# Kernel optimization log

Hardware: AMD Instinct MI355X
Metric: run time of the kernel (lower is better)

Reference implementation:

```python
import jax, jax.numpy as jnp
import numpy as np

NUM_HEADS = 16
ROPE_THETA = 10000.0


def _rope_cos_sin(head_dim, seq_len, theta=ROPE_THETA):
    # matches precompute_freqs_cis: theta ** (-(2i)/head_dim)
    exps = -(jnp.arange(0, head_dim, 2)[: head_dim // 2].astype(jnp.float32)) / head_dim
    freqs = theta ** exps                                   # [hd/2]
    ang = jnp.arange(seq_len, dtype=jnp.float32)[:, None] * freqs[None, :]  # [S, hd/2]
    return jnp.cos(ang), jnp.sin(ang)


def _apply_rope(x, cos, sin):
    # x: [B, H, S, hd]; interpret consecutive pairs as complex numbers
    x2 = x.reshape(*x.shape[:-1], -1, 2)
    xr, xi = x2[..., 0], x2[..., 1]
    c = cos[None, None]  # [1,1,S,hd/2]
    s = sin[None, None]
    outr = xr * c - xi * s
    outi = xr * s + xi * c
    return jnp.stack([outr, outi], axis=-1).reshape(x.shape)


def setup_inputs() -> dict:
    key = jax.random.key(0)
    ks = jax.random.split(key, 9)
    B, S, D = 2, 2048, 1024
    scale = 0.02
    x = jax.random.normal(ks[0], (B, S, D), jnp.float32)
    Wq = jax.random.normal(ks[1], (D, D), jnp.float32) * scale
    bq = jax.random.normal(ks[2], (D,), jnp.float32) * scale
    Wk = jax.random.normal(ks[3], (D, D), jnp.float32) * scale
    bk = jax.random.normal(ks[4], (D,), jnp.float32) * scale
    Wv = jax.random.normal(ks[5], (D, D), jnp.float32) * scale
    bv = jax.random.normal(ks[6], (D,), jnp.float32) * scale
    Wo = jax.random.normal(ks[7], (D, D), jnp.float32) * scale
    return {"x": x, "Wq": Wq, "bq": bq, "Wk": Wk, "bk": bk,
            "Wv": Wv, "bv": bv, "Wo": Wo}


def reference(x, Wq, bq, Wk, bk, Wv, bv, Wo):
    B, S, D = x.shape
    H = NUM_HEADS
    hd = D // H
    # projections (torch Linear: x @ W.T + b), split heads -> [B,H,S,hd]
    q = (x @ Wq.T + bq).reshape(B, S, H, hd).transpose(0, 2, 1, 3)
    k = (x @ Wk.T + bk).reshape(B, S, H, hd).transpose(0, 2, 1, 3)
    v = (x @ Wv.T + bv).reshape(B, S, H, hd).transpose(0, 2, 1, 3)
    cos, sin = _rope_cos_sin(hd, S)
    q = _apply_rope(q, cos, sin)
    k = _apply_rope(k, cos, sin)
    # NOTE: original scales by sqrt(input_dim), not sqrt(head_dim)
    inv_scale = 1.0 / jnp.sqrt(jnp.asarray(D, jnp.float32))
    scores = jax.nn.softmax(jnp.einsum('bhqd,bhkd->bhqk', q, k) * inv_scale, axis=-1)
    out = jnp.einsum('bhqk,bhkd->bhqd', scores, v)
    out = out.transpose(0, 2, 1, 3).reshape(B, S, D)
    return out @ Wo.T
```

## Files before the change

kernel.cpp:

```cpp
#include <hip/hip_runtime.h>
#include <math.h>

namespace {
constexpr int kB = 2;
constexpr int kS = 2048;
constexpr int kD = 1024;
constexpr int kH = 16;
constexpr int kHD = 64;
constexpr int kBS = kB * kS;
constexpr float kInvScale = 0.03125f;
constexpr float kQScale = 0.03125f * 1.4426950408889634f;
constexpr int BM = 128, BN = 64, BK = 64;
}

typedef __attribute__((ext_vector_type(8))) short short8;
typedef __attribute__((ext_vector_type(4))) float f32x4;
typedef __attribute__((ext_vector_type(4))) unsigned short u16x4;
typedef __attribute__((ext_vector_type(4))) unsigned int u32x4;

__device__ inline unsigned short f2bf(float f) {
  union { float f; unsigned u; } v;
  v.f = f;
  unsigned r = v.u + 0x7FFFu + ((v.u >> 16) & 1u);
  return (unsigned short)(r >> 16);
}

__device__ inline unsigned pack_bf16_pair(float lo, float hi) {
  union { float f; unsigned u; } a, b;
  a.f = hi; b.f = lo;
  return __builtin_amdgcn_perm(a.u + 0x8000u, b.u + 0x8000u, 0x07060302u);
}

__device__ inline void gload_lds16(const unsigned short* g, unsigned short* l) {
  __builtin_amdgcn_global_load_lds(
      (const __attribute__((address_space(1))) void*)g,
      (__attribute__((address_space(3))) void*)l, 16, 0, 0);
}

__global__ __launch_bounds__(256) void cast_prep_kernel(
    const float* __restrict__ x, const float* __restrict__ Wq,
    const float* __restrict__ Wk, const float* __restrict__ Wv,
    const float* __restrict__ Wo, unsigned short* __restrict__ xb,
    unsigned short* __restrict__ wb, float2* __restrict__ rope) {
  const int tid = blockIdx.x * 256 + threadIdx.x;
  const int stride = gridDim.x * 256;
  for (int i = tid; i < 1048576; i += stride) {
    const float* src;
    unsigned short* dst;
    int off;
    if (i < 524288) {
      src = x; dst = xb; off = i;
    } else {
      const int j = i - 524288;
      const int w = j >> 17;
      src = (w == 0) ? Wq : (w == 1) ? Wk : (w == 2) ? Wv : Wo;
      dst = wb + (size_t)w * (kD * kD);
      off = j & 131071;
    }
    const float4 a = reinterpret_cast<const float4*>(src)[off * 2];
    const float4 b = reinterpret_cast<const float4*>(src)[off * 2 + 1];
    short8 o;
    o[0] = (short)f2bf(a.x); o[1] = (short)f2bf(a.y);
    o[2] = (short)f2bf(a.z); o[3] = (short)f2bf(a.w);
    o[4] = (short)f2bf(b.x); o[5] = (short)f2bf(b.y);
    o[6] = (short)f2bf(b.z); o[7] = (short)f2bf(b.w);
    reinterpret_cast<short8*>(dst)[off] = o;
  }
  for (int i = tid; i < kS * 32; i += stride) {
    const int s = i >> 5;
    const int pr = i & 31;
    const float f = powf(10000.0f, -(float)pr / 32.0f);
    const float ang = (float)s * f;
    rope[i] = make_float2(cosf(ang), sinf(ang));
  }
}

__global__ __launch_bounds__(256) void gemm_bt_kernel(
    const unsigned short* __restrict__ A, const unsigned short* __restrict__ Wb,
    const float* __restrict__ bq, const float* __restrict__ bk,
    const float* __restrict__ bv, const float2* __restrict__ rope,
    unsigned short* __restrict__ qo, unsigned short* __restrict__ ko,
    unsigned short* __restrict__ vo, float* __restrict__ outp, int mode_base) {
  const int mode = mode_base + blockIdx.z;
  const unsigned short* __restrict__ W = Wb + (size_t)mode * (kD * kD);
  const int rt = blockIdx.x * BM;
  const int ct = blockIdx.y * BN;
  const int t = threadIdx.x;
  const int wv = t >> 6;
  const int lane = t & 63;
  const int l15 = lane & 15;
  const int lg = lane >> 4;
  const int wr = wv >> 1;
  const int wc = wv & 1;

  __shared__ unsigned short As[BM * BK];
  __shared__ unsigned short Bs[BN * BK];

  f32x4 acc[4][2];
#pragma unroll
  for (int m = 0; m < 4; ++m)
#pragma unroll
    for (int n = 0; n < 2; ++n) acc[m][n] = f32x4{0.f, 0.f, 0.f, 0.f};

  for (int kt = 0; kt < kD / BK; ++kt) {
    const int k0 = kt * BK;
    __syncthreads();
#pragma unroll
    for (int i = 0; i < 4; ++i) {
      const int off = wv * 4096 + i * 1024;
      const int p = off + lane * 16;
      const int row = p >> 7;
      const int src = ((p >> 4) & 7) ^ (row & 7);
      gload_lds16(A + (size_t)(rt + row) * kD + k0 + src * 8, As + off / 2);
    }
#pragma unroll
    for (int i = 0; i < 2; ++i) {
      const int off = wv * 2048 + i * 1024;
      const int p = off + lane * 16;
      const int row = p >> 7;
      const int src = ((p >> 4) & 7) ^ (row & 7);
      gload_lds16(W + (size_t)(ct + row) * kD + k0 + src * 8, Bs + off / 2);
    }
    __syncthreads();

#pragma unroll
    for (int ks = 0; ks < 2; ++ks) {
      short8 af[4], bf[2];
#pragma unroll
      for (int m = 0; m < 4; ++m) {
        const int row = wr * 64 + m * 16 + l15;
        const int chunk = (ks * 4 + lg) ^ (row & 7);
        af[m] = *reinterpret_cast<const short8*>(&As[row * BK + chunk * 8]);
      }
#pragma unroll
      for (int n = 0; n < 2; ++n) {
        const int row = wc * 32 + n * 16 + l15;
        const int chunk = (ks * 4 + lg) ^ (row & 7);
        bf[n] = *reinterpret_cast<const short8*>(&Bs[row * BK + chunk * 8]);
      }
      __builtin_amdgcn_s_setprio(1);
#pragma unroll
      for (int m = 0; m < 4; ++m)
#pragma unroll
        for (int n = 0; n < 2; ++n)
          acc[m][n] = __builtin_amdgcn_mfma_f32_16x16x32_bf16(
              af[m], bf[n], acc[m][n], 0, 0, 0);
      __builtin_amdgcn_s_setprio(0);
    }
  }

#pragma unroll
  for (int m = 0; m < 4; ++m) {
    const int grow0 = rt + wr * 64 + m * 16 + lg * 4;
    const int bb = grow0 >> 11;
    const int s0 = grow0 & (kS - 1);
#pragma unroll
    for (int n = 0; n < 2; ++n) {
      const int gcol = ct + wc * 32 + n * 16 + l15;
      if (mode == 3) {
#pragma unroll
        for (int reg = 0; reg < 4; ++reg)
          outp[(size_t)(grow0 + reg) * kD + gcol] = acc[m][n][reg];
      } else if (mode == 2) {
        const float bsv = bv[gcol];
        const int h = gcol >> 6, d = gcol & 63;
        u16x4 o;
#pragma unroll
        for (int reg = 0; reg < 4; ++reg)
          o[reg] = f2bf(acc[m][n][reg] + bsv);
        *reinterpret_cast<u16x4*>(
            &vo[((size_t)(bb * kH + h) * kHD + d) * kS + s0]) = o;
      } else {
        const float bsv = (mode == 0) ? bq[gcol] : bk[gcol];
        const float post = (mode == 0) ? kQScale : 1.0f;
        unsigned short* __restrict__ dst = (mode == 0) ? qo : ko;
        const int h = gcol >> 6, d = gcol & 63;
        const int pr = d >> 1;
        const float sgn = (d & 1) ? 1.0f : -1.0f;
#pragma unroll
        for (int reg = 0; reg < 4; ++reg) {
          const int s = s0 + reg;
          const float val = acc[m][n][reg] + bsv;
          const float par = __shfl_xor(val, 1);
          const float2 cs = rope[s * 32 + pr];
          const float o = (val * cs.x + par * cs.y * sgn) * post;
          dst[((size_t)(bb * kH + h) * kS + s) * kHD + d] = f2bf(o);
        }
      }
    }
  }
}

__global__ __launch_bounds__(512) void attn_mfma_kernel(
    const unsigned short* __restrict__ qb, const unsigned short* __restrict__ kb,
    const unsigned short* __restrict__ vtb, unsigned short* __restrict__ attn) {
  const int qt = blockIdx.x;
  const int h = blockIdx.y;
  const int b = blockIdx.z;
  const int t = threadIdx.x;
  const int wave = t >> 6;
  const int lane = t & 63;
  const int l15 = lane & 15;
  const int lg = lane >> 4;
  const int g = wave >> 2;
  const int st = wave & 3;

  __shared__ __align__(16) unsigned char smem[2 * 16384 + 2 * 16384 + 512];
  unsigned short* Ks0 = (unsigned short*)smem;
  unsigned short* Vs0 = (unsigned short*)(smem + 32768);
  float* Ocomb = (float*)smem;
  float* lcomb = (float*)(smem + 65536);

  const size_t bh = (size_t)(b * kH + h);
  const unsigned short* qp = qb + bh * kS * kHD;
  const unsigned short* kp = kb + bh * kS * kHD;
  const unsigned short* vp = vtb + bh * (size_t)kHD * kS;

  const int qrow0 = qt * 128 + st * 32;

  short8 qf[2][2];
#pragma unroll
  for (int qi = 0; qi < 2; ++qi)
#pragma unroll
    for (int f = 0; f < 2; ++f)
      qf[qi][f] = *reinterpret_cast<const short8*>(
          qp + (size_t)(qrow0 + qi * 16 + l15) * kHD + f * 32 + lg * 8);

  short8 ones;
#pragma unroll
  for (int j = 0; j < 8; ++j) ones[j] = (short)0x3F80;

  f32x4 acc_o[2][4], acc_l[2];
#pragma unroll
  for (int qi = 0; qi < 2; ++qi) {
    acc_l[qi] = f32x4{0.f, 0.f, 0.f, 0.f};
#pragma unroll
    for (int ot = 0; ot < 4; ++ot) acc_o[qi][ot] = f32x4{0.f, 0.f, 0.f, 0.f};
  }

  const int srow = t >> 3;
  const int sc = (t & 7) ^ (srow & 7);
  const int kvrow = (srow & 0x23) | ((srow & 0x0C) << 1) | ((srow & 0x10) >> 2);
  const int ldsoff = wave * 512;

#pragma unroll
  for (int hh = 0; hh < 2; ++hh) {
    gload_lds16(kp + (size_t)(hh * 64 + kvrow) * kHD + sc * 8,
                &Ks0[hh * 4096 + ldsoff]);
    gload_lds16(vp + (size_t)srow * kS + hh * 64 + sc * 8,
                &Vs0[hh * 4096 + ldsoff]);
  }
  __syncthreads();

  constexpr int NT = kS / 128;
  for (int kt = 0; kt < NT; ++kt) {
    const int cur = kt & 1;
    unsigned short* Ksb = Ks0 + cur * 8192;
    unsigned short* Vsb = Vs0 + cur * 8192;
    if (kt + 1 < NT) {
      const int nb = (kt + 1) * 128;
#pragma unroll
      for (int hh = 0; hh < 2; ++hh) {
        gload_lds16(kp + (size_t)(nb + hh * 64 + kvrow) * kHD + sc * 8,
                    &Ks0[(cur ^ 1) * 8192 + hh * 4096 + ldsoff]);
        gload_lds16(vp + (size_t)srow * kS + nb + hh * 64 + sc * 8,
                    &Vs0[(cur ^ 1) * 8192 + hh * 4096 + ldsoff]);
      }
    }

#pragma unroll
    for (int hh = 0; hh < 2; ++hh) {
      unsigned short* Ksc = Ksb + hh * 4096;
      unsigned short* Vsc = Vsb + hh * 4096;

      short8 kf[2][2], vf[4];
#pragma unroll
      for (int nt = 0; nt < 2; ++nt) {
        const int row = g * 32 + nt * 16 + l15;
#pragma unroll
        for (int f = 0; f < 2; ++f) {
          const int c = (f * 4 + lg) ^ (row & 7);
          kf[nt][f] = *reinterpret_cast<const short8*>(&Ksc[row * 64 + c * 8]);
        }
      }
#pragma unroll
      for (int ot = 0; ot < 4; ++ot) {
        const int row = ot * 16 + l15;
        const int c = (4 * g + lg) ^ (row & 7);
        vf[ot] = *reinterpret_cast<const short8*>(&Vsc[row * 64 + c * 8]);
      }

      f32x4 acc_s[2][2];
      __builtin_amdgcn_s_setprio(1);
#pragma unroll
      for (int qi = 0; qi < 2; ++qi)
#pragma unroll
        for (int nt = 0; nt < 2; ++nt) {
          acc_s[qi][nt] = __builtin_amdgcn_mfma_f32_16x16x32_bf16(
              kf[nt][0], qf[qi][0], f32x4{0.f, 0.f, 0.f, 0.f}, 0, 0, 0);
          acc_s[qi][nt] = __builtin_amdgcn_mfma_f32_16x16x32_bf16(
              kf[nt][1], qf[qi][1], acc_s[qi][nt], 0, 0, 0);
        }
      __builtin_amdgcn_s_setprio(0);

#pragma unroll
      for (int qi = 0; qi < 2; ++qi) {
        float p[2][4];
#pragma unroll
        for (int nt = 0; nt < 2; ++nt)
#pragma unroll
          for (int r = 0; r < 4; ++r)
            p[nt][r] = __builtin_amdgcn_exp2f(acc_s[qi][nt][r]);

        short8 pb;
        {
          u32x4 w;
          w.x = pack_bf16_pair(p[0][0], p[0][1]);
          w.y = pack_bf16_pair(p[0][2], p[0][3]);
          w.z = pack_bf16_pair(p[1][0], p[1][1]);
          w.w = pack_bf16_pair(p[1][2], p[1][3]);
          pb = *reinterpret_cast<short8*>(&w);
        }

        __builtin_amdgcn_s_setprio(1);
#pragma unroll
        for (int ot = 0; ot < 4; ++ot)
          acc_o[qi][ot] = __builtin_amdgcn_mfma_f32_16x16x32_bf16(
              vf[ot], pb, acc_o[qi][ot], 0, 0, 0);
        acc_l[qi] = __builtin_amdgcn_mfma_f32_16x16x32_bf16(
            ones, pb, acc_l[qi], 0, 0, 0);
        __builtin_amdgcn_s_setprio(0);
      }
    }

    __syncthreads();
  }

  if (g == 1) {
#pragma unroll
    for (int qi = 0; qi < 2; ++qi) {
      const int row = qi * 16 + l15;
#pragma unroll
      for (int ot = 0; ot < 4; ++ot)
        *reinterpret_cast<f32x4*>(
            &Ocomb[(st * 32 + row) * 64 + ot * 16 + lg * 4]) = acc_o[qi][ot];
      if (lg == 0) lcomb[st * 32 + row] = acc_l[qi][0];
    }
  }
  __syncthreads();
  if (g == 0) {
#pragma unroll
    for (int qi = 0; qi < 2; ++qi) {
      const int row = qi * 16 + l15;
      const float l = acc_l[qi][0] + lcomb[st * 32 + row];
      const float inv_l = 1.0f / l;
      const int s = qrow0 + row;
      unsigned short* __restrict__ dst =
          attn + ((size_t)b * kS + s) * kD + h * kHD;
#pragma unroll
      for (int ot = 0; ot < 4; ++ot) {
        const f32x4 oth = *reinterpret_cast<const f32x4*>(
            &Ocomb[(st * 32 + row) * 64 + ot * 16 + lg * 4]);
        u16x4 o;
        o[0] = f2bf((acc_o[qi][ot][0] + oth[0]) * inv_l);
        o[1] = f2bf((acc_o[qi][ot][1] + oth[1]) * inv_l);
        o[2] = f2bf((acc_o[qi][ot][2] + oth[2]) * inv_l);
        o[3] = f2bf((acc_o[qi][ot][3] + oth[3]) * inv_l);
        *reinterpret_cast<u16x4*>(&dst[ot * 16 + lg * 4]) = o;
      }
    }
  }
}

extern "C" void kernel_launch(void* const* d_in, const int* in_sizes, int n_in,
                              void* d_out, int out_size, void* d_ws,
                              size_t ws_size, hipStream_t stream) {
  (void)in_sizes; (void)n_in; (void)out_size; (void)ws_size;
  const float* x = (const float*)d_in[0];
  const float* Wq = (const float*)d_in[1];
  const float* bq = (const float*)d_in[2];
  const float* Wk = (const float*)d_in[3];
  const float* bk = (const float*)d_in[4];
  const float* Wv = (const float*)d_in[5];
  const float* bv = (const float*)d_in[6];
  const float* Wo = (const float*)d_in[7];
  float* out = (float*)d_out;

  const size_t n = (size_t)kBS * kD;
  float2* rope = (float2*)d_ws;
  unsigned short* xb = (unsigned short*)(rope + kS * 32);
  unsigned short* wb = xb + n;
  unsigned short* qb = wb + 4 * (size_t)kD * kD;
  unsigned short* kb = qb + n;
  unsigned short* vt = kb + n;
  unsigned short* attnb = vt + n;

  cast_prep_kernel<<<2048, 256, 0, stream>>>(x, Wq, Wk, Wv, Wo, xb, wb, rope);

  dim3 gq(kBS / BM, kD / BN, 3);
  gemm_bt_kernel<<<gq, dim3(256), 0, stream>>>(xb, wb, bq, bk, bv, rope, qb,
                                               kb, vt, nullptr, 0);

  dim3 ga(kS / 128, kH, kB);
  attn_mfma_kernel<<<ga, dim3(512), 0, stream>>>(qb, kb, vt, attnb);

  dim3 go(kBS / BM, kD / BN, 1);
  gemm_bt_kernel<<<go, dim3(256), 0, stream>>>(attnb, wb, bq, bk, bv, rope, qb,
                                               kb, vt, out, 3);
}
```

Baseline: 106.0 us.

## Fuse Q/K/V projections into one kernel sharing the activation tile

Replaces the three-way grid-z QKV GEMM with a single kernel where each block loads the activation tile once and multiplies it against the Q, K and V weight tiles, keeping three accumulator sets. The output projection gets its own specialized kernel with no mode branching. This removes redundant activation loads and per-block mode dispatch, at the cost of more registers and LDS per block and a third as many blocks, which may reduce occupancy and parallelism.

```diff
diff --git a/kernel.cpp b/kernel.cpp
--- a/kernel.cpp
+++ b/kernel.cpp
@@ -75,14 +75,12 @@
   }
 }
 
-__global__ __launch_bounds__(256) void gemm_bt_kernel(
+__global__ __launch_bounds__(256) void qkv_fused_kernel(
     const unsigned short* __restrict__ A, const unsigned short* __restrict__ Wb,
     const float* __restrict__ bq, const float* __restrict__ bk,
     const float* __restrict__ bv, const float2* __restrict__ rope,
     unsigned short* __restrict__ qo, unsigned short* __restrict__ ko,
-    unsigned short* __restrict__ vo, float* __restrict__ outp, int mode_base) {
-  const int mode = mode_base + blockIdx.z;
-  const unsigned short* __restrict__ W = Wb + (size_t)mode * (kD * kD);
+    unsigned short* __restrict__ vo) {
   const int rt = blockIdx.x * BM;
   const int ct = blockIdx.y * BN;
   const int t = threadIdx.x;
@@ -94,13 +92,15 @@
   const int wc = wv & 1;
 
   __shared__ unsigned short As[BM * BK];
-  __shared__ unsigned short Bs[BN * BK];
-
-  f32x4 acc[4][2];
-#pragma unroll
-  for (int m = 0; m < 4; ++m)
-#pragma unroll
-    for (int n = 0; n < 2; ++n) acc[m][n] = f32x4{0.f, 0.f, 0.f, 0.f};
+  __shared__ unsigned short Bs[3][BN * BK];
+
+  f32x4 acc[3][4][2];
+#pragma unroll
+  for (int m3 = 0; m3 < 3; ++m3)
+#pragma unroll
+    for (int m = 0; m < 4; ++m)
+#pragma unroll
+      for (int n = 0; n < 2; ++n) acc[m3][m][n] = f32x4{0.f, 0.f, 0.f, 0.f};
 
   for (int kt = 0; kt < kD / BK; ++kt) {
     const int k0 = kt * BK;
@@ -114,6 +114,124 @@
       gload_lds16(A + (size_t)(rt + row) * kD + k0 + src * 8, As + off / 2);
     }
 #pragma unroll
+    for (int m3 = 0; m3 < 3; ++m3)
+#pragma unroll
+      for (int i = 0; i < 2; ++i) {
+        const int off = wv * 2048 + i * 1024;
+        const int p = off + lane * 16;
+        const int row = p >> 7;
+        const int src = ((p >> 4) & 7) ^ (row & 7);
+        gload_lds16(Wb + (size_t)m3 * (kD * kD) + (size_t)(ct + row) * kD +
+                        k0 + src * 8,
+                    &Bs[m3][off / 2]);
+      }
+    __syncthreads();
+
+#pragma unroll
+    for (int ks = 0; ks < 2; ++ks) {
+      short8 af[4], bf[3][2];
+#pragma unroll
+      for (int m = 0; m < 4; ++m) {
+        const int row = wr * 64 + m * 16 + l15;
+        const int chunk = (ks * 4 + lg) ^ (row & 7);
+        af[m] = *reinterpret_cast<const short8*>(&As[row * BK + chunk * 8]);
+      }
+#pragma unroll
+      for (int m3 = 0; m3 < 3; ++m3)
+#pragma unroll
+        for (int n = 0; n < 2; ++n) {
+          const int row = wc * 32 + n * 16 + l15;
+          const int chunk = (ks * 4 + lg) ^ (row & 7);
+          bf[m3][n] =
+              *reinterpret_cast<const short8*>(&Bs[m3][row * BK + chunk * 8]);
+        }
+      __builtin_amdgcn_s_setprio(1);
+#pragma unroll
+      for (int m3 = 0; m3 < 3; ++m3)
+#pragma unroll
+        for (int m = 0; m < 4; ++m)
+#pragma unroll
+          for (int n = 0; n < 2; ++n)
+            acc[m3][m][n] = __builtin_amdgcn_mfma_f32_16x16x32_bf16(
+                af[m], bf[m3][n], acc[m3][m][n], 0, 0, 0);
+      __builtin_amdgcn_s_setprio(0);
+    }
+  }
+
+#pragma unroll
+  for (int m = 0; m < 4; ++m) {
+    const int grow0 = rt + wr * 64 + m * 16 + lg * 4;
+    const int bb = grow0 >> 11;
+    const int s0 = grow0 & (kS - 1);
+#pragma unroll
+    for (int n = 0; n < 2; ++n) {
+      const int gcol = ct + wc * 32 + n * 16 + l15;
+      const int h = gcol >> 6, d = gcol & 63;
+      {
+        const float bsv = bv[gcol];
+        u16x4 o;
+#pragma unroll
+        for (int reg = 0; reg < 4; ++reg)
+          o[reg] = f2bf(acc[2][m][n][reg] + bsv);
+        *reinterpret_cast<u16x4*>(
+            &vo[((size_t)(bb * kH + h) * kHD + d) * kS + s0]) = o;
+      }
+      const int pr = d >> 1;
+      const float sgn = (d & 1) ? 1.0f : -1.0f;
+#pragma unroll
+      for (int m3 = 0; m3 < 2; ++m3) {
+        const float bsv = (m3 == 0) ? bq[gcol] : bk[gcol];
+        const float post = (m3 == 0) ? kQScale : 1.0f;
+        unsigned short* __restrict__ dst = (m3 == 0) ? qo : ko;
+#pragma unroll
+        for (int reg = 0; reg < 4; ++reg) {
+          const int s = s0 + reg;
+          const float val = acc[m3][m][n][reg] + bsv;
+          const float par = __shfl_xor(val, 1);
+          const float2 cs = rope[s * 32 + pr];
+          const float o = (val * cs.x + par * cs.y * sgn) * post;
+          dst[((size_t)(bb * kH + h) * kS + s) * kHD + d] = f2bf(o);
+        }
+      }
+    }
+  }
+}
+
+__global__ __launch_bounds__(256) void out_proj_kernel(
+    const unsigned short* __restrict__ A, const unsigned short* __restrict__ Wb,
+    float* __restrict__ outp) {
+  const unsigned short* __restrict__ W = Wb + (size_t)3 * (kD * kD);
+  const int rt = blockIdx.x * BM;
+  const int ct = blockIdx.y * BN;
+  const int t = threadIdx.x;
+  const int wv = t >> 6;
+  const int lane = t & 63;
+  const int l15 = lane & 15;
+  const int lg = lane >> 4;
+  const int wr = wv >> 1;
+  const int wc = wv & 1;
+
+  __shared__ unsigned short As[BM * BK];
+  __shared__ unsigned short Bs[BN * BK];
+
+  f32x4 acc[4][2];
+#pragma unroll
+  for (int m = 0; m < 4; ++m)
+#pragma unroll
+    for (int n = 0; n < 2; ++n) acc[m][n] = f32x4{0.f, 0.f, 0.f, 0.f};
+
+  for (int kt = 0; kt < kD / BK; ++kt) {
+    const int k0 = kt * BK;
+    __syncthreads();
+#pragma unroll
+    for (int i = 0; i < 4; ++i) {
+      const int off = wv * 4096 + i * 1024;
+      const int p = off + lane * 16;
+      const int row = p >> 7;
+      const int src = ((p >> 4) & 7) ^ (row & 7);
+      gload_lds16(A + (size_t)(rt + row) * kD + k0 + src * 8, As + off / 2);
+    }
+#pragma unroll
     for (int i = 0; i < 2; ++i) {
       const int off = wv * 2048 + i * 1024;
       const int p = off + lane * 16;
@@ -152,41 +270,12 @@
 #pragma unroll
   for (int m = 0; m < 4; ++m) {
     const int grow0 = rt + wr * 64 + m * 16 + lg * 4;
-    const int bb = grow0 >> 11;
-    const int s0 = grow0 & (kS - 1);
 #pragma unroll
     for (int n = 0; n < 2; ++n) {
       const int gcol = ct + wc * 32 + n * 16 + l15;
-      if (mode == 3) {
-#pragma unroll
-        for (int reg = 0; reg < 4; ++reg)
-          outp[(size_t)(grow0 + reg) * kD + gcol] = acc[m][n][reg];
-      } else if (mode == 2) {
-        const float bsv = bv[gcol];
-        const int h = gcol >> 6, d = gcol & 63;
-        u16x4 o;
-#pragma unroll
-        for (int reg = 0; reg < 4; ++reg)
-          o[reg] = f2bf(acc[m][n][reg] + bsv);
-        *reinterpret_cast<u16x4*>(
-            &vo[((size_t)(bb * kH + h) * kHD + d) * kS + s0]) = o;
-      } else {
-        const float bsv = (mode == 0) ? bq[gcol] : bk[gcol];
-        const float post = (mode == 0) ? kQScale : 1.0f;
-        unsigned short* __restrict__ dst = (mode == 0) ? qo : ko;
-        const int h = gcol >> 6, d = gcol & 63;
-        const int pr = d >> 1;
-        const float sgn = (d & 1) ? 1.0f : -1.0f;
-#pragma unroll
-        for (int reg = 0; reg < 4; ++reg) {
-          const int s = s0 + reg;
-          const float val = acc[m][n][reg] + bsv;
-          const float par = __shfl_xor(val, 1);
-          const float2 cs = rope[s * 32 + pr];
-          const float o = (val * cs.x + par * cs.y * sgn) * post;
-          dst[((size_t)(bb * kH + h) * kS + s) * kHD + d] = f2bf(o);
-        }
-      }
+#pragma unroll
+      for (int reg = 0; reg < 4; ++reg)
+        outp[(size_t)(grow0 + reg) * kD + gcol] = acc[m][n][reg];
     }
   }
 }
@@ -397,14 +486,13 @@
 
   cast_prep_kernel<<<2048, 256, 0, stream>>>(x, Wq, Wk, Wv, Wo, xb, wb, rope);
 
-  dim3 gq(kBS / BM, kD / BN, 3);
-  gemm_bt_kernel<<<gq, dim3(256), 0, stream>>>(xb, wb, bq, bk, bv, rope, qb,
-                                               kb, vt, nullptr, 0);
+  dim3 gq(kBS / BM, kD / BN);
+  qkv_fused_kernel<<<gq, dim3(256), 0, stream>>>(xb, wb, bq, bk, bv, rope, qb,
+                                                 kb, vt);
 
   dim3 ga(kS / 128, kH, kB);
   attn_mfma_kernel<<<ga, dim3(512), 0, stream>>>(qb, kb, vt, attnb);
 
-  dim3 go(kBS / BM, kD / BN, 1);
-  gemm_bt_kernel<<<go, dim3(256), 0, stream>>>(attnb, wb, bq, bk, bv, rope, qb,
-                                               kb, vt, out, 3);
-}
+  dim3 go(kBS / BM, kD / BN);
+  out_proj_kernel<<<go, dim3(256), 0, stream>>>(attnb, wb, out);
+}
```

New measurement: 122.1 us. 15.2% more time.
